# Kernel optimization log

Measured on AMD Instinct MI355X. Metric: run time of the kernel, lower is better.

## Reference

```python
import jax, jax.numpy as jnp
import numpy as np

N = 100000          # active voxels
KS = 7              # kernel size per spatial dim
K = KS ** 3         # 343 kernel offsets
G = 64              # voxel grid extent
INPLANES = 128
PLANES = 128
D2 = PLANES // 4    # 32
EPS = 1e-5


def _build_neighbor_map(seed=0):
    # Random distinct voxel coordinates in a G^3 grid, then for every point and
    # every 7^3 offset find the index of the neighboring voxel (-1 if absent).
    rng = np.random.default_rng(seed)
    lin = rng.choice(G ** 3, size=N, replace=False)
    coords = np.stack(np.unravel_index(lin, (G, G, G)), axis=1).astype(np.int64)  # [N,3]
    keys = coords[:, 0] * G * G + coords[:, 1] * G + coords[:, 2]
    order = np.argsort(keys)
    skeys = keys[order]
    offs = np.arange(KS) - KS // 2
    off_grid = np.stack(np.meshgrid(offs, offs, offs, indexing='ij'), axis=-1).reshape(K, 3)
    q = coords[:, None, :] + off_grid[None, :, :]          # [N,K,3]
    inb = np.all((q >= 0) & (q < G), axis=-1)
    qk = q[..., 0] * G * G + q[..., 1] * G + q[..., 2]
    pos = np.searchsorted(skeys, qk)
    pos_c = np.clip(pos, 0, N - 1)
    found = inb & (skeys[pos_c] == qk)
    nbr = np.where(found, order[pos_c], -1).astype(np.int32)  # [N,K]
    return jnp.asarray(nbr)


def setup_inputs() -> dict:
    key = jax.random.key(0)
    k = jax.random.split(key, 4)
    feats = jax.random.normal(k[0], (N, INPLANES), jnp.float32)
    w1 = jax.random.normal(k[1], (INPLANES, D2), jnp.float32) / np.sqrt(INPLANES)
    w_conv = jax.random.normal(k[2], (K, D2, D2), jnp.float32) / np.sqrt(K * D2)
    w2 = jax.random.normal(k[3], (D2, PLANES), jnp.float32) / np.sqrt(D2)
    return {
        'feats': feats,
        'nbr': _build_neighbor_map(),
        'w1': w1,
        'ln1_g': jnp.ones((D2,), jnp.float32),
        'ln1_b': jnp.zeros((D2,), jnp.float32),
        'w_conv': w_conv,
        'w2': w2,
        'ln2_g': jnp.ones((PLANES,), jnp.float32),
        'ln2_b': jnp.zeros((PLANES,), jnp.float32),
    }


def _layernorm(x, g, b):
    m = jnp.mean(x, axis=-1, keepdims=True)
    v = jnp.var(x, axis=-1, keepdims=True)
    return (x - m) * jax.lax.rsqrt(v + EPS) * g + b


def _sparse_conv(x, nbr, w):
    # x: [N,d2], nbr: [N,K], w: [K,d2,d2]; gather-apply-scatter per kernel offset.
    def step(acc, inp):
        idx, wk = inp                                # idx: [N], wk: [d2,d2]
        valid = (idx >= 0).astype(x.dtype)[:, None]
        g = jnp.take(x, jnp.maximum(idx, 0), axis=0) * valid
        return acc + g @ wk, None
    acc0 = jnp.zeros((x.shape[0], w.shape[2]), x.dtype)
    out, _ = jax.lax.scan(step, acc0, (nbr.T, w))
    return out


def reference(feats, nbr, w1, ln1_g, ln1_b, w_conv, w2, ln2_g, ln2_b):
    shortcut = feats                                  # inplanes == planes -> Identity
    h = _layernorm(feats @ w1, ln1_g, ln1_b)          # unary_1: [N,d2]
    h = _sparse_conv(h, nbr, w_conv)                  # 7^3 sparse conv: [N,d2]
    h = _layernorm(h @ w2, ln2_g, ln2_b)              # unary_2: [N,planes]
    h = jax.nn.gelu(h, approximate=False)             # drop_path is Identity (rate 0)
    return h + shortcut
```

## Files before the change

kernel.cpp:

```cpp
#include <hip/hip_runtime.h>
#include <hip/hip_bf16.h>

#define N_PTS 100000
#define KOFF 343
#define EPS 1e-5f
#define NTILES 3125
#define SSTRIDE 87

typedef __hip_bfloat16 bf16;
typedef __attribute__((ext_vector_type(4))) float f32x4;
typedef __attribute__((ext_vector_type(16))) float f32x16;
typedef __attribute__((ext_vector_type(8))) short s16x8;

__global__ __launch_bounds__(256) void pack_kernel(const float* __restrict__ w_conv,
                                                   bf16* __restrict__ wpk) {
  int t = blockIdx.x * 256 + threadIdx.x;
  if (t >= KOFF * 128) return;
  int l = t & 63;
  int s = (t >> 6) & 1;
  int k = t >> 7;
  int col = l & 31;
  int kq = l >> 5;
  const float* wk = w_conv + k * 1024;
  s16x8 v;
  for (int j = 0; j < 8; ++j) {
    bf16 h = __float2bfloat16(wk[(s * 16 + kq * 8 + j) * 32 + col]);
    short sv;
    __builtin_memcpy(&sv, &h, 2);
    v[j] = sv;
  }
  *reinterpret_cast<s16x8*>(reinterpret_cast<char*>(wpk) + (size_t)t * 16) = v;
}

__global__ __launch_bounds__(256) void unary1_kernel(const float* __restrict__ feats,
    const float* __restrict__ w1, const float* __restrict__ g1,
    const float* __restrict__ b1, bf16* __restrict__ h1b) {
  __shared__ float sf[8][128];
  __shared__ float sw[128 * 32];
  int tid = threadIdx.x;
  int rbase = blockIdx.x * 8;
  if (blockIdx.x == 0 && tid < 16)
    reinterpret_cast<int*>(h1b)[N_PTS * 16 + tid] = 0;
  for (int i = tid; i < 1024; i += 256)
    reinterpret_cast<f32x4*>(sw)[i] = reinterpret_cast<const f32x4*>(w1)[i];
  {
    int i = tid;
    int r = rbase + (i >> 5);
    f32x4 v = reinterpret_cast<const f32x4*>(feats)[(size_t)r * 32 + (i & 31)];
    reinterpret_cast<f32x4*>(&sf[0][0])[i] = v;
  }
  __syncthreads();
  int half = tid >> 5;
  int c = tid & 31;
  int r = rbase + half;
  const float* frow = sf[half];
  float acc = 0.f;
  #pragma unroll 8
  for (int kk = 0; kk < 128; ++kk)
    acc += frow[kk] * sw[kk * 32 + c];
  float s = acc, s2 = acc * acc;
  #pragma unroll
  for (int m = 16; m >= 1; m >>= 1) {
    s  += __shfl_xor(s,  m, 64);
    s2 += __shfl_xor(s2, m, 64);
  }
  float mean = s * (1.f / 32.f);
  float var  = s2 * (1.f / 32.f) - mean * mean;
  float y = (acc - mean) * rsqrtf(var + EPS) * g1[c] + b1[c];
  h1b[(size_t)r * 32 + c] = __float2bfloat16(y);
}

template<int KCNT, int KBASE>
__device__ __forceinline__ void stage_round(const int* __restrict__ g,
                                            int* __restrict__ snbr, int wave, int l) {
  #pragma unroll
  for (int rr = 0; rr < 8; ++rr) {
    int row = wave * 8 + rr;
    const int* src = g + row * KOFF + KBASE;
    if (l < KCNT) {
      int v = src[l];
      snbr[row * SSTRIDE + l] = v < 0 ? N_PTS : v;
    }
    if (64 + l < KCNT) {
      int v = src[64 + l];
      snbr[row * SSTRIDE + 64 + l] = v < 0 ? N_PTS : v;
    }
  }
}

template<int KCNT, int KBASE>
__device__ __forceinline__ void process_round(const int* __restrict__ snbr,
    const bf16* __restrict__ h1b, const s16x8* __restrict__ wb,
    f32x16& acc, int wave, int l, int col, int kq) {
  int k0 = (KCNT * wave) >> 2;
  int k1 = (KCNT * (wave + 1)) >> 2;
  const int* myrow = snbr + col * SSTRIDE;
  int id[4];
  #pragma unroll
  for (int j = 0; j < 4; ++j) id[j] = (k0 + j < k1) ? myrow[k0 + j] : N_PTS;
  for (int kb = k0; kb < k1; kb += 4) {
    s16x8 A0[4], A1[4], B0[4], B1[4];
    #pragma unroll
    for (int j = 0; j < 4; ++j) {
      const s16x8* r = reinterpret_cast<const s16x8*>(h1b + (size_t)id[j] * 32);
      A0[j] = r[kq];
      A1[j] = r[2 + kq];
      int kc = (kb + j < k1) ? kb + j : k1 - 1;
      B0[j] = wb[(size_t)(KBASE + kc) * 128 + l];
      B1[j] = wb[(size_t)(KBASE + kc) * 128 + 64 + l];
    }
    int idn[4];
    #pragma unroll
    for (int j = 0; j < 4; ++j) idn[j] = (kb + 4 + j < k1) ? myrow[kb + 4 + j] : N_PTS;
    #pragma unroll
    for (int j = 0; j < 4; ++j) {
      acc = __builtin_amdgcn_mfma_f32_32x32x16_bf16(A0[j], B0[j], acc, 0, 0, 0);
      acc = __builtin_amdgcn_mfma_f32_32x32x16_bf16(A1[j], B1[j], acc, 0, 0, 0);
    }
    #pragma unroll
    for (int j = 0; j < 4; ++j) id[j] = idn[j];
  }
}

__global__ __launch_bounds__(256, 4) void conv_s2_kernel(const bf16* __restrict__ h1b,
    const int* __restrict__ nbr, const bf16* __restrict__ wpk,
    float* __restrict__ h2) {
  __shared__ int sbuf[4096];
  int tid = threadIdx.x;
  int wave = tid >> 6;
  int l = tid & 63;
  int col = l & 31;
  int kq = l >> 5;
  int pbase = blockIdx.x * 32;
  const int* g = nbr + (size_t)pbase * KOFF;
  const s16x8* wb = reinterpret_cast<const s16x8*>(wpk);
  f32x16 acc;
  #pragma unroll
  for (int i = 0; i < 16; ++i) acc[i] = 0.f;

  stage_round<86, 0>(g, sbuf, wave, l);
  __syncthreads();
  process_round<86, 0>(sbuf, h1b, wb, acc, wave, l, col, kq);
  __syncthreads();
  stage_round<86, 86>(g, sbuf, wave, l);
  __syncthreads();
  process_round<86, 86>(sbuf, h1b, wb, acc, wave, l, col, kq);
  __syncthreads();
  stage_round<86, 172>(g, sbuf, wave, l);
  __syncthreads();
  process_round<86, 172>(sbuf, h1b, wb, acc, wave, l, col, kq);
  __syncthreads();
  stage_round<85, 258>(g, sbuf, wave, l);
  __syncthreads();
  process_round<85, 258>(sbuf, h1b, wb, acc, wave, l, col, kq);
  __syncthreads();

  float* red = reinterpret_cast<float*>(sbuf);
  #pragma unroll
  for (int reg = 0; reg < 16; ++reg) {
    int rrow = (reg & 3) + 8 * (reg >> 2) + 4 * kq;
    red[wave * 1024 + rrow * 32 + col] = acc[reg];
  }
  __syncthreads();
  const f32x4* rv = reinterpret_cast<const f32x4*>(red);
  f32x4 s = rv[tid] + rv[256 + tid] + rv[512 + tid] + rv[768 + tid];
  reinterpret_cast<f32x4*>(h2 + (size_t)pbase * 32)[tid] = s;
}

__global__ __launch_bounds__(256) void unary2_kernel(const float* __restrict__ h2,
    const float* __restrict__ w2, const float* __restrict__ g2,
    const float* __restrict__ b2, const float* __restrict__ feats,
    float* __restrict__ out) {
  int tid = threadIdx.x;
  int wave = tid >> 6;
  int l = tid & 63;
  int r = blockIdx.x * 4 + wave;
  const float* hrow = h2 + (size_t)r * 32;
  float acc0 = 0.f, acc1 = 0.f;
  #pragma unroll
  for (int q = 0; q < 8; ++q) {
    f32x4 hv = reinterpret_cast<const f32x4*>(hrow)[q];
    #pragma unroll
    for (int j = 0; j < 4; ++j) {
      int kk = q * 4 + j;
      float h = hv[j];
      acc0 += h * w2[kk * 128 + l];
      acc1 += h * w2[kk * 128 + 64 + l];
    }
  }
  float s = acc0 + acc1, s2 = acc0 * acc0 + acc1 * acc1;
  #pragma unroll
  for (int m = 32; m >= 1; m >>= 1) {
    s  += __shfl_xor(s,  m, 64);
    s2 += __shfl_xor(s2, m, 64);
  }
  float mean = s * (1.f / 128.f);
  float var  = s2 * (1.f / 128.f) - mean * mean;
  float inv = rsqrtf(var + EPS);
  float y0 = (acc0 - mean) * inv * g2[l] + b2[l];
  float y1 = (acc1 - mean) * inv * g2[64 + l] + b2[64 + l];
  float ge0 = 0.5f * y0 * (1.f + erff(y0 * 0.70710678118f));
  float ge1 = 0.5f * y1 * (1.f + erff(y1 * 0.70710678118f));
  out[(size_t)r * 128 + l]      = ge0 + feats[(size_t)r * 128 + l];
  out[(size_t)r * 128 + 64 + l] = ge1 + feats[(size_t)r * 128 + 64 + l];
}

extern "C" void kernel_launch(void* const* d_in, const int* in_sizes, int n_in,
                              void* d_out, int out_size, void* d_ws, size_t ws_size,
                              hipStream_t stream) {
  const float* feats  = (const float*)d_in[0];
  const int*   nbr    = (const int*)d_in[1];
  const float* w1     = (const float*)d_in[2];
  const float* ln1_g  = (const float*)d_in[3];
  const float* ln1_b  = (const float*)d_in[4];
  const float* w_conv = (const float*)d_in[5];
  const float* w2     = (const float*)d_in[6];
  const float* ln2_g  = (const float*)d_in[7];
  const float* ln2_b  = (const float*)d_in[8];
  float* out = (float*)d_out;
  char* ws = (char*)d_ws;
  bf16*  h1b = (bf16*)ws;
  bf16*  wpk = (bf16*)(ws + 6400064);
  float* h2  = (float*)(ws + 7102528);

  hipLaunchKernelGGL(pack_kernel,    dim3((KOFF * 128 + 255) / 256), dim3(256), 0, stream, w_conv, wpk);
  hipLaunchKernelGGL(unary1_kernel,  dim3(N_PTS / 8),                dim3(256), 0, stream, feats, w1, ln1_g, ln1_b, h1b);
  hipLaunchKernelGGL(conv_s2_kernel, dim3(NTILES),                   dim3(256), 0, stream, h1b, nbr, wpk, h2);
  hipLaunchKernelGGL(unary2_kernel,  dim3(N_PTS / 4),                dim3(256), 0, stream, h2, w2, ln2_g, ln2_b, feats, out);
}
```

Measured before the change: 386.1 us.

## Process two 32-point tiles per 512-thread block with fewer staging rounds

The sparse conv kernel now uses 8 waves per block covering 64 points (two 32-point tiles). Each group of four waves splits the kernel offsets for one tile. Neighbor indices are staged in two rounds of about 172 offsets instead of four rounds of 86, which halves the barrier count. Waves on both tiles read the same packed weights, so those loads can be reused through cache. In exchange, staging now does a per-element integer division with a flat loop, LDS per block grows to about 44KB, and a bounds check is needed for the odd final tile.

New measurement: 376.1 us. -2.6%, faster.

```diff
diff --git a/kernel.cpp b/kernel.cpp
--- a/kernel.cpp
+++ b/kernel.cpp
@@ -5,7 +5,7 @@
 #define KOFF 343
 #define EPS 1e-5f
 #define NTILES 3125
-#define SSTRIDE 87
+#define RSTRIDE 173
 
 typedef __hip_bfloat16 bf16;
 typedef __attribute__((ext_vector_type(4))) float f32x4;
@@ -71,30 +71,24 @@
 }
 
 template<int KCNT, int KBASE>
-__device__ __forceinline__ void stage_round(const int* __restrict__ g,
-                                            int* __restrict__ snbr, int wave, int l) {
-  #pragma unroll
-  for (int rr = 0; rr < 8; ++rr) {
-    int row = wave * 8 + rr;
-    const int* src = g + row * KOFF + KBASE;
-    if (l < KCNT) {
-      int v = src[l];
-      snbr[row * SSTRIDE + l] = v < 0 ? N_PTS : v;
-    }
-    if (64 + l < KCNT) {
-      int v = src[64 + l];
-      snbr[row * SSTRIDE + 64 + l] = v < 0 ? N_PTS : v;
-    }
+__device__ __forceinline__ void stage_round(const int* __restrict__ nbr,
+    int* __restrict__ sbuf, int tid, int pbase0) {
+  for (int i = tid; i < 64 * KCNT; i += 512) {
+    int row = i / KCNT;
+    int kk = i - row * KCNT;
+    int p = pbase0 + row;
+    int v = (p < N_PTS) ? nbr[(size_t)p * KOFF + KBASE + kk] : -1;
+    sbuf[row * RSTRIDE + kk] = v < 0 ? N_PTS : v;
   }
 }
 
 template<int KCNT, int KBASE>
-__device__ __forceinline__ void process_round(const int* __restrict__ snbr,
+__device__ __forceinline__ void process_round(const int* __restrict__ sbuf,
     const bf16* __restrict__ h1b, const s16x8* __restrict__ wb,
-    f32x16& acc, int wave, int l, int col, int kq) {
-  int k0 = (KCNT * wave) >> 2;
-  int k1 = (KCNT * (wave + 1)) >> 2;
-  const int* myrow = snbr + col * SSTRIDE;
+    f32x16& acc, int wsub, int l, int col, int kq, int tilesel) {
+  int k0 = (KCNT * wsub) >> 2;
+  int k1 = (KCNT * (wsub + 1)) >> 2;
+  const int* myrow = sbuf + (tilesel * 32 + col) * RSTRIDE;
   int id[4];
   #pragma unroll
   for (int j = 0; j < 4; ++j) id[j] = (k0 + j < k1) ? myrow[k0 + j] : N_PTS;
@@ -122,37 +116,30 @@
   }
 }
 
-__global__ __launch_bounds__(256, 4) void conv_s2_kernel(const bf16* __restrict__ h1b,
+__global__ __launch_bounds__(512) void conv_w8_kernel(const bf16* __restrict__ h1b,
     const int* __restrict__ nbr, const bf16* __restrict__ wpk,
     float* __restrict__ h2) {
-  __shared__ int sbuf[4096];
+  __shared__ int sbuf[64 * RSTRIDE];
   int tid = threadIdx.x;
   int wave = tid >> 6;
+  int wsub = wave & 3;
+  int tilesel = wave >> 2;
   int l = tid & 63;
   int col = l & 31;
   int kq = l >> 5;
-  int pbase = blockIdx.x * 32;
-  const int* g = nbr + (size_t)pbase * KOFF;
+  int pbase0 = blockIdx.x * 64;
   const s16x8* wb = reinterpret_cast<const s16x8*>(wpk);
   f32x16 acc;
   #pragma unroll
   for (int i = 0; i < 16; ++i) acc[i] = 0.f;
 
-  stage_round<86, 0>(g, sbuf, wave, l);
-  __syncthreads();
-  process_round<86, 0>(sbuf, h1b, wb, acc, wave, l, col, kq);
-  __syncthreads();
-  stage_round<86, 86>(g, sbuf, wave, l);
-  __syncthreads();
-  process_round<86, 86>(sbuf, h1b, wb, acc, wave, l, col, kq);
-  __syncthreads();
-  stage_round<86, 172>(g, sbuf, wave, l);
-  __syncthreads();
-  process_round<86, 172>(sbuf, h1b, wb, acc, wave, l, col, kq);
-  __syncthreads();
-  stage_round<85, 258>(g, sbuf, wave, l);
-  __syncthreads();
-  process_round<85, 258>(sbuf, h1b, wb, acc, wave, l, col, kq);
+  stage_round<172, 0>(nbr, sbuf, tid, pbase0);
+  __syncthreads();
+  process_round<172, 0>(sbuf, h1b, wb, acc, wsub, l, col, kq, tilesel);
+  __syncthreads();
+  stage_round<171, 172>(nbr, sbuf, tid, pbase0);
+  __syncthreads();
+  process_round<171, 172>(sbuf, h1b, wb, acc, wsub, l, col, kq, tilesel);
   __syncthreads();
 
   float* red = reinterpret_cast<float*>(sbuf);
@@ -163,8 +150,12 @@
   }
   __syncthreads();
   const f32x4* rv = reinterpret_cast<const f32x4*>(red);
-  f32x4 s = rv[tid] + rv[256 + tid] + rv[512 + tid] + rv[768 + tid];
-  reinterpret_cast<f32x4*>(h2 + (size_t)pbase * 32)[tid] = s;
+  int t = tid >> 8;
+  int e = tid & 255;
+  f32x4 s = rv[t * 1024 + e] + rv[t * 1024 + 256 + e]
+          + rv[t * 1024 + 512 + e] + rv[t * 1024 + 768 + e];
+  if (pbase0 + (t + 1) * 32 <= N_PTS)
+    reinterpret_cast<f32x4*>(h2 + (size_t)pbase0 * 32)[tid] = s;
 }
 
 __global__ __launch_bounds__(256) void unary2_kernel(const float* __restrict__ h2,
@@ -225,6 +216,6 @@
 
   hipLaunchKernelGGL(pack_kernel,    dim3((KOFF * 128 + 255) / 256), dim3(256), 0, stream, w_conv, wpk);
   hipLaunchKernelGGL(unary1_kernel,  dim3(N_PTS / 8),                dim3(256), 0, stream, feats, w1, ln1_g, ln1_b, h1b);
-  hipLaunchKernelGGL(conv_s2_kernel, dim3(NTILES),                   dim3(256), 0, stream, h1b, nbr, wpk, h2);
+  hipLaunchKernelGGL(conv_w8_kernel, dim3((NTILES + 1) / 2),         dim3(512), 0, stream, h1b, nbr, wpk, h2);
   hipLaunchKernelGGL(unary2_kernel,  dim3(N_PTS / 4),                dim3(256), 0, stream, h2, w2, ln2_g, ln2_b, feats, out);
 }
```
